# Optimization experiments

Hardware: AMD Instinct MI355X
Metric: run time of the kernel (lower is better)

Reference implementation:

```python
import jax, jax.numpy as jnp
import numpy as np

D_MODEL = 1024
N_HEADS = 16
HEAD_DIM = D_MODEL // N_HEADS  # 64
BATCH, SEQ = 2, 2048
MASK_FILL = -1000000000.0


def setup_inputs() -> dict:
    key = jax.random.key(0)
    ks = jax.random.split(key, 13)
    s = 1.0 / np.sqrt(D_MODEL)
    inp = {
        "q": jax.random.normal(ks[0], (BATCH, SEQ, D_MODEL), jnp.float32),
        "k": jax.random.normal(ks[1], (BATCH, SEQ, D_MODEL), jnp.float32),
        "v": jax.random.normal(ks[2], (BATCH, SEQ, D_MODEL), jnp.float32),
        "mask": jax.random.randint(ks[3], (BATCH, 1, SEQ, SEQ), 0, 2, jnp.int32),
        "Wq": jax.random.normal(ks[4], (D_MODEL, D_MODEL), jnp.float32) * s,
        "bq": jax.random.normal(ks[5], (D_MODEL,), jnp.float32) * s,
        "Wk": jax.random.normal(ks[6], (D_MODEL, D_MODEL), jnp.float32) * s,
        "bk": jax.random.normal(ks[7], (D_MODEL,), jnp.float32) * s,
        "Wv": jax.random.normal(ks[8], (D_MODEL, D_MODEL), jnp.float32) * s,
        "bv": jax.random.normal(ks[9], (D_MODEL,), jnp.float32) * s,
        "Wo": jax.random.normal(ks[10], (D_MODEL, D_MODEL), jnp.float32) * s,
        "bo": jax.random.normal(ks[11], (D_MODEL,), jnp.float32) * s,
    }
    return inp


def reference(q, k, v, mask, Wq, bq, Wk, bk, Wv, bv, Wo, bo):
    batch, seq, feat = q.shape
    # Linear projections (torch Linear: x @ W.T + b)
    qp = q @ Wq.T + bq
    kp = k @ Wk.T + bk
    vp = v @ Wv.T + bv

    def split(x):
        # (B, S, D) -> (B, H, S, Dh)
        return x.reshape(batch, seq, N_HEADS, HEAD_DIM).swapaxes(1, 2)

    qh, kh, vh = split(qp), split(kp), split(vp)

    # (B, H, S, S) score matrix, scaled
    score = jnp.einsum("bhqd,bhkd->bhqk", qh, kh) / jnp.sqrt(
        jnp.asarray(HEAD_DIM, qh.dtype))
    score = jnp.where(mask == 0, jnp.asarray(MASK_FILL, score.dtype), score)
    attn = jax.nn.softmax(score, axis=-1)
    out = jnp.einsum("bhqk,bhkd->bhqd", attn, vh)  # (B, H, S, Dh)
    joint = out.swapaxes(1, 2).reshape(batch, seq, feat)
    return joint @ Wo.T + bo
```

## Files before the change

### kernel.cpp

```cpp
#include <hip/hip_runtime.h>

typedef unsigned short u16;
typedef unsigned int u32;
typedef unsigned long long u64;
typedef float f32x4 __attribute__((ext_vector_type(4)));
typedef float f32x16 __attribute__((ext_vector_type(16)));
typedef __bf16 bf16x4 __attribute__((ext_vector_type(4)));
typedef __bf16 bf16x8 __attribute__((ext_vector_type(8)));
typedef u16 u16x8 __attribute__((ext_vector_type(8)));
typedef u32 u32x4 __attribute__((ext_vector_type(4)));

#define QSCALE 0.18033688011112042f

__device__ __forceinline__ u16 f2bf(float f) {
  unsigned int u = __float_as_uint(f);
  u += 0x7fffu + ((u >> 16) & 1u);
  return (u16)(u >> 16);
}

__device__ __forceinline__ void async16(const void* g, void* l) {
  __builtin_amdgcn_global_load_lds(
      (__attribute__((address_space(1))) void*)g,
      (__attribute__((address_space(3))) void*)l,
      16, 0, 0);
}

__device__ __forceinline__ f32x4 mfma16(bf16x8 a, bf16x8 b, f32x4 c) {
  return __builtin_amdgcn_mfma_f32_16x16x32_bf16(a, b, c, 0, 0, 0);
}

__device__ __forceinline__ f32x16 mfma32(bf16x8 a, bf16x8 b, f32x16 c) {
  return __builtin_amdgcn_mfma_f32_32x32x16_bf16(a, b, c, 0, 0, 0);
}

__device__ __forceinline__ u32 cvtpk(float lo, float hi) {
  u32 r;
  asm("v_cvt_pk_bf16_f32 %0, %1, %2" : "=v"(r) : "v"(lo), "v"(hi));
  return r;
}

__device__ __forceinline__ void pswap(u32& a, u32& b) {
  asm("v_permlane32_swap_b32 %0, %1" : "+v"(a), "+v"(b));
}

struct CvtArgs {
  const float* src[7];
  u16* dst[7];
};

__global__ __launch_bounds__(256) void cvt_kernel(CvtArgs a) {
  int z = blockIdx.z;
  int n = (z < 3) ? 4194304 : 1048576;
  int base = (blockIdx.x * 256 + threadIdx.x) * 8;
  if (base >= n) return;
  const float* s = a.src[z] + base;
  f32x4 x0 = *(const f32x4*)s;
  f32x4 x1 = *(const f32x4*)(s + 4);
  u16x8 pk;
  pk[0]=f2bf(x0[0]); pk[1]=f2bf(x0[1]); pk[2]=f2bf(x0[2]); pk[3]=f2bf(x0[3]);
  pk[4]=f2bf(x1[0]); pk[5]=f2bf(x1[1]); pk[6]=f2bf(x1[2]); pk[7]=f2bf(x1[3]);
  *(u16x8*)(a.dst[z] + base) = pk;
}

__global__ __launch_bounds__(256) void pack_mask_kernel(
    const int* __restrict__ mask, u64* __restrict__ pm) {
  int idx = blockIdx.x * 256 + threadIdx.x;
  const int4* src = (const int4*)(mask + (size_t)idx * 64);
  u64 bits = 0ull;
#pragma unroll
  for (int j = 0; j < 16; ++j) {
    int4 v = src[j];
    if (v.x) bits |= 1ull << (4 * j + 0);
    if (v.y) bits |= 1ull << (4 * j + 1);
    if (v.z) bits |= 1ull << (4 * j + 2);
    if (v.w) bits |= 1ull << (4 * j + 3);
  }
  pm[idx] = bits;
}

__device__ __forceinline__ void gemm_body(const u16* __restrict__ A,
                                          const u16* __restrict__ W,
                                          const float* __restrict__ bias,
                                          void* __restrict__ outraw, int mode,
                                          float oscale, int m0, int n0) {
  alignas(16) __shared__ u16 lA[128 * 32];
  alignas(16) __shared__ u16 lB[128 * 32];
  const int tid = threadIdx.x;
  const int lane = tid & 63, wv = tid >> 6;
  const int wm = wv >> 1, wn = wv & 1;
  const int l15 = lane & 15, quad = lane >> 4;
  const int srow = lane >> 2;
  const int scol = (lane & 3) * 8;

  f32x4 acc[4][4] = {};

  for (int k0 = 0; k0 < 1024; k0 += 32) {
#pragma unroll
    for (int t = 0; t < 2; ++t) {
      int rb = (wv * 2 + t) * 16;
      async16(A + (size_t)(m0 + rb + srow) * 1024 + k0 + scol, (char*)lA + rb * 64);
      async16(W + (size_t)(n0 + rb + srow) * 1024 + k0 + scol, (char*)lB + rb * 64);
    }
    __syncthreads();
    bf16x8 af[4], bfr[4];
#pragma unroll
    for (int i = 0; i < 4; ++i) {
      af[i]  = *(const bf16x8*)(lA + (wm * 64 + i * 16 + l15) * 32 + quad * 8);
      bfr[i] = *(const bf16x8*)(lB + (wn * 64 + i * 16 + l15) * 32 + quad * 8);
    }
#pragma unroll
    for (int i = 0; i < 4; ++i)
#pragma unroll
      for (int j = 0; j < 4; ++j)
        acc[i][j] = mfma16(af[i], bfr[j], acc[i][j]);
    __syncthreads();
  }

#pragma unroll
  for (int i = 0; i < 4; ++i) {
    int mbase = m0 + wm * 64 + i * 16 + quad * 4;
#pragma unroll
    for (int j = 0; j < 4; ++j) {
      int n = n0 + wn * 64 + j * 16 + l15;
      float bv = bias[n];
#pragma unroll
      for (int r = 0; r < 4; ++r) {
        int m = mbase + r;
        if (mode == 0) {
          float val = (acc[i][j][r] + bv) * oscale;
          int b = m >> 11, s = m & 2047, h = n >> 6, dh = n & 63;
          ((u16*)outraw)[((((size_t)b * 16 + h) * 2048 + s) << 6) + dh] = f2bf(val);
        } else if (mode == 1) {
          float val = (acc[i][j][r] + bias[m]) * oscale;
          int h = m >> 6, dh = m & 63, b = n >> 11, s = n & 2047;
          ((u16*)outraw)[((((size_t)b * 16 + h) * 64 + dh) << 11) + s] = f2bf(val);
        } else {
          float val = (acc[i][j][r] + bv) * oscale;
          ((float*)outraw)[(size_t)m * 1024 + n] = val;
        }
      }
    }
  }
}

__global__ __launch_bounds__(256) void gemm_qkv_kernel(
    const u16* __restrict__ qb, const u16* __restrict__ kb, const u16* __restrict__ vb,
    const u16* __restrict__ Wqb, const float* __restrict__ bq,
    const u16* __restrict__ Wkb, const float* __restrict__ bk,
    const u16* __restrict__ Wvb, const float* __restrict__ bv,
    u16* __restrict__ qp, u16* __restrict__ kp, u16* __restrict__ vt) {
  if (blockIdx.z == 0)
    gemm_body(qb, Wqb, bq, qp, 0, QSCALE, blockIdx.y * 128, blockIdx.x * 128);
  else if (blockIdx.z == 1)
    gemm_body(kb, Wkb, bk, kp, 0, 1.0f, blockIdx.y * 128, blockIdx.x * 128);
  else
    gemm_body(Wvb, vb, bv, vt, 1, 1.0f, blockIdx.x * 128, blockIdx.y * 128);
}

__global__ __launch_bounds__(256) void gemm_o_kernel(
    const u16* __restrict__ joint, const u16* __restrict__ Wob,
    const float* __restrict__ bo, float* __restrict__ out) {
  gemm_body(joint, Wob, bo, out, 2, 1.0f, blockIdx.y * 128, blockIdx.x * 128);
}

__global__ __launch_bounds__(512, 2) void attn_kernel(
    const u16* __restrict__ qp, const u16* __restrict__ kp,
    const u16* __restrict__ vt, const u64* __restrict__ pm,
    u16* __restrict__ joint) {
  alignas(16) __shared__ char smem[32768];

  const int tid = threadIdx.x, lane = tid & 63, wv = tid >> 6;
  const int l31 = lane & 31, hi = lane >> 5, l7 = lane & 7;
  const int qg = wv >> 1, kh = wv & 1;

  const int bid = blockIdx.x;
  const int grp = ((bid & 7) << 2) | ((bid >> 3) & 3);
  const int q0 = (bid >> 5) * 128;
  const int hd = grp & 15, b = grp >> 4;

  const size_t head_off = ((size_t)b * 16 + hd) * 2048 * 64;
  const u16* Qh = qp + head_off;
  const u16* Kh = kp + head_off;
  const u16* Vh = vt + head_off;
  const int qr = q0 + qg * 32 + l31;
  const u32* pmq32 = (const u32*)(pm + ((size_t)b * 2048 + qr) * 32) + kh;

  bf16x8 qf[4];
  {
    const u16* qrow = Qh + (size_t)qr * 64 + hi * 8;
#pragma unroll
    for (int d = 0; d < 4; ++d) qf[d] = *(const bf16x8*)(qrow + d * 16);
  }

  const int sd = tid;
  const int kr = sd >> 3, ks = ((sd & 7) ^ (kr & 7)) * 8;
  const u16* kg = Kh + (size_t)kr * 64 + ks;
  const u16* vg = Vh + (size_t)kr * 2048 + ks;

  f32x16 O[2] = {};
  f32x4 lacc = {};
  const f32x16 fz16 = {};

  async16(kg, smem + sd * 16);
  async16(vg, smem + 16384 + sd * 16);

  for (int kt = 0; kt < 32; ++kt) {
    __syncthreads();

    if (kt != 31) {
      const size_t kadv = (size_t)(kt + 1) * 4096;
      const int vadv = (kt + 1) * 64;
      char* kd = smem + (((kt + 1) & 1) << 13);
      char* vd = smem + 16384 + (((kt + 1) & 1) << 13);
      async16(kg + kadv, kd + sd * 16);
      async16(vg + vadv, vd + sd * 16);
    }

    u32 wh = pmq32[2 * kt];
    const char* kc = smem + ((kt & 1) << 13);
    const char* vc = smem + 16384 + ((kt & 1) << 13);

    bf16x8 kf[4];
#pragma unroll
    for (int d = 0; d < 4; ++d)
      kf[d] = *(const bf16x8*)(kc + (kh * 32 + l31) * 128 +
                               (((2 * d + hi) ^ l7) << 4));

    f32x16 S;
    {
      __builtin_amdgcn_s_setprio(1);
      f32x16 s = mfma32(kf[0], qf[0], fz16);
      s = mfma32(kf[1], qf[1], s);
      s = mfma32(kf[2], qf[2], s);
      S = mfma32(kf[3], qf[3], s);
      __builtin_amdgcn_s_setprio(0);
    }

    bf16x8 vf[2][2];
#pragma unroll
    for (int g = 0; g < 2; ++g)
#pragma unroll
      for (int t = 0; t < 2; ++t) {
        int vks = kh * 2 + t;
        vf[g][t] = *(const bf16x8*)(vc + (g * 32 + l31) * 128 +
                                    (((2 * vks + hi) ^ l7) << 4));
      }

    {
      const int hi4 = hi * 4;
#pragma unroll
      for (int rq = 0; rq < 4; ++rq) {
        u32 nib = wh >> (rq * 8 + hi4);
#pragma unroll
        for (int r4 = 0; r4 < 4; ++r4) {
          int i = rq * 4 + r4;
          float pe = __builtin_amdgcn_exp2f(S[i]);
          S[i] = ((nib >> r4) & 1u) ? pe : 0.f;
        }
        f32x4 sv = {S[rq * 4 + 0], S[rq * 4 + 1], S[rq * 4 + 2], S[rq * 4 + 3]};
        lacc += sv;
      }
    }

    bf16x8 pf[2];
#pragma unroll
    for (int t = 0; t < 2; ++t) {
      int ra = t * 8;
      u32 w0a = cvtpk(S[ra + 0], S[ra + 1]);
      u32 w1a = cvtpk(S[ra + 2], S[ra + 3]);
      u32 w0b = cvtpk(S[ra + 4], S[ra + 5]);
      u32 w1b = cvtpk(S[ra + 6], S[ra + 7]);
      pswap(w0a, w0b);
      pswap(w1a, w1b);
      u32x4 tt = {w0a, w1a, w0b, w1b};
      pf[t] = __builtin_bit_cast(bf16x8, tt);
    }

    __builtin_amdgcn_s_setprio(1);
#pragma unroll
    for (int g = 0; g < 2; ++g) {
      f32x16 o = O[g];
      o = mfma32(vf[g][0], pf[0], o);
      O[g] = mfma32(vf[g][1], pf[1], o);
    }
    __builtin_amdgcn_s_setprio(0);
  }

  float lp = (lacc[0] + lacc[1]) + (lacc[2] + lacc[3]);
  lp += __shfl_xor(lp, 32, 64);
  __syncthreads();
  float* exch = (float*)smem;
  float* e = exch + (qg * 64 + lane) * 17;
  if (kh == 1) {
#pragma unroll
    for (int i = 0; i < 16; ++i) e[i] = O[0][i];
    e[16] = lp;
  }
  __syncthreads();
  if (kh == 0) {
#pragma unroll
    for (int i = 0; i < 16; ++i) O[0][i] += e[i];
    lp += e[16];
  }
  __syncthreads();
  if (kh == 1) {
#pragma unroll
    for (int i = 0; i < 16; ++i) e[i] = O[1][i];
  }
  __syncthreads();
  if (kh == 0) {
#pragma unroll
    for (int i = 0; i < 16; ++i) O[1][i] += e[i];
    float inv = 1.0f / lp;
    size_t row_off = ((size_t)b * 2048 + qr) * 1024 + hd * 64;
#pragma unroll
    for (int g = 0; g < 2; ++g)
#pragma unroll
      for (int rq = 0; rq < 4; ++rq) {
        f32x4 ov = {O[g][rq * 4 + 0] * inv, O[g][rq * 4 + 1] * inv,
                    O[g][rq * 4 + 2] * inv, O[g][rq * 4 + 3] * inv};
        bf16x4 obv = __builtin_convertvector(ov, bf16x4);
        *(u64*)(joint + row_off + g * 32 + rq * 8 + hi * 4) =
            *(const u64*)&obv;
      }
  }
}

extern "C" void kernel_launch(void* const* d_in, const int* in_sizes, int n_in,
                              void* d_out, int out_size, void* d_ws, size_t ws_size,
                              hipStream_t stream) {
  const float* q  = (const float*)d_in[0];
  const float* k  = (const float*)d_in[1];
  const float* v  = (const float*)d_in[2];
  const int* mask = (const int*)d_in[3];
  const float* Wq = (const float*)d_in[4];
  const float* bq = (const float*)d_in[5];
  const float* Wk = (const float*)d_in[6];
  const float* bk = (const float*)d_in[7];
  const float* Wv = (const float*)d_in[8];
  const float* bv = (const float*)d_in[9];
  const float* Wo = (const float*)d_in[10];
  const float* bo = (const float*)d_in[11];
  float* out = (float*)d_out;

  u16* w = (u16*)d_ws;
  u16* qp    = w;
  u16* kp    = w + 4194304;
  u16* vt    = w + 8388608;
  u16* qb    = w + 12582912;
  u16* kb    = w + 16777216;
  u16* vb    = w + 20971520;
  u16* Wqb   = w + 25165824;
  u16* Wkb   = w + 26214400;
  u16* Wvb   = w + 27262976;
  u16* Wob   = w + 28311552;
  u64* pm    = (u64*)(w + 29360128);
  u16* joint = qb;

  CvtArgs ca;
  ca.src[0] = q;  ca.dst[0] = qb;
  ca.src[1] = k;  ca.dst[1] = kb;
  ca.src[2] = v;  ca.dst[2] = vb;
  ca.src[3] = Wq; ca.dst[3] = Wqb;
  ca.src[4] = Wk; ca.dst[4] = Wkb;
  ca.src[5] = Wv; ca.dst[5] = Wvb;
  ca.src[6] = Wo; ca.dst[6] = Wob;

  pack_mask_kernel<<<dim3(512), dim3(256), 0, stream>>>(mask, pm);
  cvt_kernel<<<dim3(2048, 1, 7), dim3(256), 0, stream>>>(ca);
  gemm_qkv_kernel<<<dim3(8, 32, 3), dim3(256), 0, stream>>>(
      qb, kb, vb, Wqb, bq, Wkb, bk, Wvb, bv, qp, kp, vt);
  attn_kernel<<<dim3(512), dim3(512), 0, stream>>>(qp, kp, vt, pm, joint);
  gemm_o_kernel<<<dim3(8, 32, 1), dim3(256), 0, stream>>>(joint, Wob, bo, out);
}
```

Measured before the change: 272.7 us.

## Fuse all stages into one cooperative persistent megakernel with grid syncs

Replaces the five separate launches (mask pack, bf16 convert, QKV GEMM, attention, output GEMM) with one cooperative kernel that runs each stage as a grid-stride loop and separates stages with grid.sync. The GEMM tile is shrunk to 128x128 per 512-thread block (each wave computes 32x64) so it matches the attention block shape. The aim is to remove per-launch overhead and inter-kernel gaps. In exchange it pays for grid barriers, gives the GEMMs 512-thread blocks with a smaller per-wave tile, and limits occupancy to what a cooperative launch allows.

```diff
diff --git a/kernel.cpp b/kernel.cpp
--- a/kernel.cpp
+++ b/kernel.cpp
@@ -1,4 +1,7 @@
 #include <hip/hip_runtime.h>
+#include <hip/hip_cooperative_groups.h>
+
+namespace cg = cooperative_groups;
 
 typedef unsigned short u16;
 typedef unsigned int u32;
@@ -43,73 +46,46 @@
   asm("v_permlane32_swap_b32 %0, %1" : "+v"(a), "+v"(b));
 }
 
-struct CvtArgs {
-  const float* src[7];
-  u16* dst[7];
+struct MegaArgs {
+  const float* csrc[7];
+  u16* cdst[7];
+  const int* mask;
+  u64* pm;
+  const float *bq, *bk, *bv, *bo;
+  u16 *qp, *kp, *vt, *joint;
+  float* out;
 };
 
-__global__ __launch_bounds__(256) void cvt_kernel(CvtArgs a) {
-  int z = blockIdx.z;
-  int n = (z < 3) ? 4194304 : 1048576;
-  int base = (blockIdx.x * 256 + threadIdx.x) * 8;
-  if (base >= n) return;
-  const float* s = a.src[z] + base;
-  f32x4 x0 = *(const f32x4*)s;
-  f32x4 x1 = *(const f32x4*)(s + 4);
-  u16x8 pk;
-  pk[0]=f2bf(x0[0]); pk[1]=f2bf(x0[1]); pk[2]=f2bf(x0[2]); pk[3]=f2bf(x0[3]);
-  pk[4]=f2bf(x1[0]); pk[5]=f2bf(x1[1]); pk[6]=f2bf(x1[2]); pk[7]=f2bf(x1[3]);
-  *(u16x8*)(a.dst[z] + base) = pk;
-}
-
-__global__ __launch_bounds__(256) void pack_mask_kernel(
-    const int* __restrict__ mask, u64* __restrict__ pm) {
-  int idx = blockIdx.x * 256 + threadIdx.x;
-  const int4* src = (const int4*)(mask + (size_t)idx * 64);
-  u64 bits = 0ull;
-#pragma unroll
-  for (int j = 0; j < 16; ++j) {
-    int4 v = src[j];
-    if (v.x) bits |= 1ull << (4 * j + 0);
-    if (v.y) bits |= 1ull << (4 * j + 1);
-    if (v.z) bits |= 1ull << (4 * j + 2);
-    if (v.w) bits |= 1ull << (4 * j + 3);
-  }
-  pm[idx] = bits;
-}
-
-__device__ __forceinline__ void gemm_body(const u16* __restrict__ A,
+__device__ __forceinline__ void gemm_tile(const u16* __restrict__ A,
                                           const u16* __restrict__ W,
                                           const float* __restrict__ bias,
                                           void* __restrict__ outraw, int mode,
-                                          float oscale, int m0, int n0) {
-  alignas(16) __shared__ u16 lA[128 * 32];
-  alignas(16) __shared__ u16 lB[128 * 32];
+                                          float oscale, int m0, int n0,
+                                          char* lds) {
+  u16* lA = (u16*)lds;
+  u16* lB = (u16*)(lds + 8192);
   const int tid = threadIdx.x;
   const int lane = tid & 63, wv = tid >> 6;
   const int wm = wv >> 1, wn = wv & 1;
   const int l15 = lane & 15, quad = lane >> 4;
-  const int srow = lane >> 2;
-  const int scol = (lane & 3) * 8;
-
-  f32x4 acc[4][4] = {};
+  const int srow = tid >> 2;
+  const int scol = (tid & 3) * 8;
+
+  f32x4 acc[2][4] = {};
 
   for (int k0 = 0; k0 < 1024; k0 += 32) {
-#pragma unroll
-    for (int t = 0; t < 2; ++t) {
-      int rb = (wv * 2 + t) * 16;
-      async16(A + (size_t)(m0 + rb + srow) * 1024 + k0 + scol, (char*)lA + rb * 64);
-      async16(W + (size_t)(n0 + rb + srow) * 1024 + k0 + scol, (char*)lB + rb * 64);
-    }
-    __syncthreads();
-    bf16x8 af[4], bfr[4];
-#pragma unroll
-    for (int i = 0; i < 4; ++i) {
-      af[i]  = *(const bf16x8*)(lA + (wm * 64 + i * 16 + l15) * 32 + quad * 8);
-      bfr[i] = *(const bf16x8*)(lB + (wn * 64 + i * 16 + l15) * 32 + quad * 8);
-    }
-#pragma unroll
-    for (int i = 0; i < 4; ++i)
+    async16(A + (size_t)(m0 + srow) * 1024 + k0 + scol, lds + tid * 16);
+    async16(W + (size_t)(n0 + srow) * 1024 + k0 + scol, lds + 8192 + tid * 16);
+    __syncthreads();
+    bf16x8 af[2], bfr[4];
+#pragma unroll
+    for (int i = 0; i < 2; ++i)
+      af[i] = *(const bf16x8*)(lA + (wm * 32 + i * 16 + l15) * 32 + quad * 8);
+#pragma unroll
+    for (int j = 0; j < 4; ++j)
+      bfr[j] = *(const bf16x8*)(lB + (wn * 64 + j * 16 + l15) * 32 + quad * 8);
+#pragma unroll
+    for (int i = 0; i < 2; ++i)
 #pragma unroll
       for (int j = 0; j < 4; ++j)
         acc[i][j] = mfma16(af[i], bfr[j], acc[i][j]);
@@ -117,8 +93,8 @@
   }
 
 #pragma unroll
-  for (int i = 0; i < 4; ++i) {
-    int mbase = m0 + wm * 64 + i * 16 + quad * 4;
+  for (int i = 0; i < 2; ++i) {
+    int mbase = m0 + wm * 32 + i * 16 + quad * 4;
 #pragma unroll
     for (int j = 0; j < 4; ++j) {
       int n = n0 + wn * 64 + j * 16 + l15;
@@ -131,11 +107,11 @@
           int b = m >> 11, s = m & 2047, h = n >> 6, dh = n & 63;
           ((u16*)outraw)[((((size_t)b * 16 + h) * 2048 + s) << 6) + dh] = f2bf(val);
         } else if (mode == 1) {
-          float val = (acc[i][j][r] + bias[m]) * oscale;
+          float val = acc[i][j][r] + bias[m];
           int h = m >> 6, dh = m & 63, b = n >> 11, s = n & 2047;
           ((u16*)outraw)[((((size_t)b * 16 + h) * 64 + dh) << 11) + s] = f2bf(val);
         } else {
-          float val = (acc[i][j][r] + bv) * oscale;
+          float val = acc[i][j][r] + bv;
           ((float*)outraw)[(size_t)m * 1024 + n] = val;
         }
       }
@@ -143,233 +119,271 @@
   }
 }
 
-__global__ __launch_bounds__(256) void gemm_qkv_kernel(
-    const u16* __restrict__ qb, const u16* __restrict__ kb, const u16* __restrict__ vb,
-    const u16* __restrict__ Wqb, const float* __restrict__ bq,
-    const u16* __restrict__ Wkb, const float* __restrict__ bk,
-    const u16* __restrict__ Wvb, const float* __restrict__ bv,
-    u16* __restrict__ qp, u16* __restrict__ kp, u16* __restrict__ vt) {
-  if (blockIdx.z == 0)
-    gemm_body(qb, Wqb, bq, qp, 0, QSCALE, blockIdx.y * 128, blockIdx.x * 128);
-  else if (blockIdx.z == 1)
-    gemm_body(kb, Wkb, bk, kp, 0, 1.0f, blockIdx.y * 128, blockIdx.x * 128);
-  else
-    gemm_body(Wvb, vb, bv, vt, 1, 1.0f, blockIdx.x * 128, blockIdx.y * 128);
-}
-
-__global__ __launch_bounds__(256) void gemm_o_kernel(
-    const u16* __restrict__ joint, const u16* __restrict__ Wob,
-    const float* __restrict__ bo, float* __restrict__ out) {
-  gemm_body(joint, Wob, bo, out, 2, 1.0f, blockIdx.y * 128, blockIdx.x * 128);
-}
-
-__global__ __launch_bounds__(512, 2) void attn_kernel(
-    const u16* __restrict__ qp, const u16* __restrict__ kp,
-    const u16* __restrict__ vt, const u64* __restrict__ pm,
-    u16* __restrict__ joint) {
+__global__ __launch_bounds__(512, 2) void mega_kernel(MegaArgs a) {
   alignas(16) __shared__ char smem[32768];
-
-  const int tid = threadIdx.x, lane = tid & 63, wv = tid >> 6;
-  const int l31 = lane & 31, hi = lane >> 5, l7 = lane & 7;
-  const int qg = wv >> 1, kh = wv & 1;
-
-  const int bid = blockIdx.x;
-  const int grp = ((bid & 7) << 2) | ((bid >> 3) & 3);
-  const int q0 = (bid >> 5) * 128;
-  const int hd = grp & 15, b = grp >> 4;
-
-  const size_t head_off = ((size_t)b * 16 + hd) * 2048 * 64;
-  const u16* Qh = qp + head_off;
-  const u16* Kh = kp + head_off;
-  const u16* Vh = vt + head_off;
-  const int qr = q0 + qg * 32 + l31;
-  const u32* pmq32 = (const u32*)(pm + ((size_t)b * 2048 + qr) * 32) + kh;
-
-  bf16x8 qf[4];
+  cg::grid_group grid = cg::this_grid();
+  const int G = gridDim.x;
+  const int tid = threadIdx.x;
+
   {
-    const u16* qrow = Qh + (size_t)qr * 64 + hi * 8;
-#pragma unroll
-    for (int d = 0; d < 4; ++d) qf[d] = *(const bf16x8*)(qrow + d * 16);
-  }
-
-  const int sd = tid;
-  const int kr = sd >> 3, ks = ((sd & 7) ^ (kr & 7)) * 8;
-  const u16* kg = Kh + (size_t)kr * 64 + ks;
-  const u16* vg = Vh + (size_t)kr * 2048 + ks;
-
-  f32x16 O[2] = {};
-  f32x4 lacc = {};
-  const f32x16 fz16 = {};
-
-  async16(kg, smem + sd * 16);
-  async16(vg, smem + 16384 + sd * 16);
-
-  for (int kt = 0; kt < 32; ++kt) {
-    __syncthreads();
-
-    if (kt != 31) {
-      const size_t kadv = (size_t)(kt + 1) * 4096;
-      const int vadv = (kt + 1) * 64;
-      char* kd = smem + (((kt + 1) & 1) << 13);
-      char* vd = smem + 16384 + (((kt + 1) & 1) << 13);
-      async16(kg + kadv, kd + sd * 16);
-      async16(vg + vadv, vd + sd * 16);
-    }
-
-    u32 wh = pmq32[2 * kt];
-    const char* kc = smem + ((kt & 1) << 13);
-    const char* vc = smem + 16384 + ((kt & 1) << 13);
-
-    bf16x8 kf[4];
-#pragma unroll
-    for (int d = 0; d < 4; ++d)
-      kf[d] = *(const bf16x8*)(kc + (kh * 32 + l31) * 128 +
-                               (((2 * d + hi) ^ l7) << 4));
-
-    f32x16 S;
+    const int gtid = blockIdx.x * 512 + tid;
+    const int gstr = G * 512;
+    for (int i = gtid; i < 2097152; i += gstr) {
+      int z, off;
+      if (i < 1572864) { z = i >> 19; off = (i & 524287) * 8; }
+      else { int j = i - 1572864; z = 3 + (j >> 17); off = (j & 131071) * 8; }
+      const float* s = a.csrc[z] + off;
+      f32x4 x0 = *(const f32x4*)s;
+      f32x4 x1 = *(const f32x4*)(s + 4);
+      u16x8 pk;
+      pk[0]=f2bf(x0[0]); pk[1]=f2bf(x0[1]); pk[2]=f2bf(x0[2]); pk[3]=f2bf(x0[3]);
+      pk[4]=f2bf(x1[0]); pk[5]=f2bf(x1[1]); pk[6]=f2bf(x1[2]); pk[7]=f2bf(x1[3]);
+      *(u16x8*)(a.cdst[z] + off) = pk;
+    }
+    for (int i = gtid; i < 131072; i += gstr) {
+      const int4* src = (const int4*)(a.mask + (size_t)i * 64);
+      u64 bits = 0ull;
+#pragma unroll
+      for (int j = 0; j < 16; ++j) {
+        int4 v = src[j];
+        if (v.x) bits |= 1ull << (4 * j + 0);
+        if (v.y) bits |= 1ull << (4 * j + 1);
+        if (v.z) bits |= 1ull << (4 * j + 2);
+        if (v.w) bits |= 1ull << (4 * j + 3);
+      }
+      a.pm[i] = bits;
+    }
+  }
+  __threadfence();
+  grid.sync();
+
+  for (int job = blockIdx.x; job < 768; job += G) {
+    int z = job >> 8, t = job & 255;
+    int my = (t >> 3) * 128, nx = (t & 7) * 128;
+    if (z == 0)
+      gemm_tile(a.cdst[0], a.cdst[3], a.bq, a.qp, 0, QSCALE, my, nx, smem);
+    else if (z == 1)
+      gemm_tile(a.cdst[1], a.cdst[4], a.bk, a.kp, 0, 1.0f, my, nx, smem);
+    else
+      gemm_tile(a.cdst[5], a.cdst[2], a.bv, a.vt, 1, 1.0f, nx, my, smem);
+  }
+  __threadfence();
+  grid.sync();
+
+  for (int bid = blockIdx.x; bid < 512; bid += G) {
+    __syncthreads();
+    const int lane = tid & 63, wv = tid >> 6;
+    const int l31 = lane & 31, hi = lane >> 5, l7 = lane & 7;
+    const int qg = wv >> 1, kh = wv & 1;
+
+    const int grp = ((bid & 7) << 2) | ((bid >> 3) & 3);
+    const int q0 = (bid >> 5) * 128;
+    const int hd = grp & 15, b = grp >> 4;
+
+    const size_t head_off = ((size_t)b * 16 + hd) * 2048 * 64;
+    const u16* Qh = a.qp + head_off;
+    const u16* Kh = a.kp + head_off;
+    const u16* Vh = a.vt + head_off;
+    const int qr = q0 + qg * 32 + l31;
+    const u32* pmq32 = (const u32*)(a.pm + ((size_t)b * 2048 + qr) * 32) + kh;
+
+    bf16x8 qf[4];
     {
+      const u16* qrow = Qh + (size_t)qr * 64 + hi * 8;
+#pragma unroll
+      for (int d = 0; d < 4; ++d) qf[d] = *(const bf16x8*)(qrow + d * 16);
+    }
+
+    const int sd = tid;
+    const int kr = sd >> 3, ks = ((sd & 7) ^ (kr & 7)) * 8;
+    const u16* kg = Kh + (size_t)kr * 64 + ks;
+    const u16* vg = Vh + (size_t)kr * 2048 + ks;
+
+    f32x16 O[2] = {};
+    f32x4 lacc = {};
+    const f32x16 fz16 = {};
+
+    async16(kg, smem + sd * 16);
+    async16(vg, smem + 16384 + sd * 16);
+
+    for (int kt = 0; kt < 32; ++kt) {
+      __syncthreads();
+
+      if (kt != 31) {
+        const size_t kadv = (size_t)(kt + 1) * 4096;
+        const int vadv = (kt + 1) * 64;
+        char* kd = smem + (((kt + 1) & 1) << 13);
+        char* vd = smem + 16384 + (((kt + 1) & 1) << 13);
+        async16(kg + kadv, kd + sd * 16);
+        async16(vg + vadv, vd + sd * 16);
+      }
+
+      u32 wh = pmq32[2 * kt];
+      const char* kc = smem + ((kt & 1) << 13);
+      const char* vc = smem + 16384 + ((kt & 1) << 13);
+
+      bf16x8 kf[4];
+#pragma unroll
+      for (int d = 0; d < 4; ++d)
+        kf[d] = *(const bf16x8*)(kc + (kh * 32 + l31) * 128 +
+                                 (((2 * d + hi) ^ l7) << 4));
+
+      f32x16 S;
+      {
+        __builtin_amdgcn_s_setprio(1);
+        f32x16 s = mfma32(kf[0], qf[0], fz16);
+        s = mfma32(kf[1], qf[1], s);
+        s = mfma32(kf[2], qf[2], s);
+        S = mfma32(kf[3], qf[3], s);
+        __builtin_amdgcn_s_setprio(0);
+      }
+
+      bf16x8 vf[2][2];
+#pragma unroll
+      for (int g = 0; g < 2; ++g)
+#pragma unroll
+        for (int t = 0; t < 2; ++t) {
+          int vks = kh * 2 + t;
+          vf[g][t] = *(const bf16x8*)(vc + (g * 32 + l31) * 128 +
+                                      (((2 * vks + hi) ^ l7) << 4));
+        }
+
+      {
+        const int hi4 = hi * 4;
+#pragma unroll
+        for (int rq = 0; rq < 4; ++rq) {
+          u32 nib = wh >> (rq * 8 + hi4);
+#pragma unroll
+          for (int r4 = 0; r4 < 4; ++r4) {
+            int i = rq * 4 + r4;
+            float pe = __builtin_amdgcn_exp2f(S[i]);
+            S[i] = ((nib >> r4) & 1u) ? pe : 0.f;
+          }
+          f32x4 sv = {S[rq * 4 + 0], S[rq * 4 + 1], S[rq * 4 + 2], S[rq * 4 + 3]};
+          lacc += sv;
+        }
+      }
+
+      bf16x8 pf[2];
+#pragma unroll
+      for (int t = 0; t < 2; ++t) {
+        int ra = t * 8;
+        u32 w0a = cvtpk(S[ra + 0], S[ra + 1]);
+        u32 w1a = cvtpk(S[ra + 2], S[ra + 3]);
+        u32 w0b = cvtpk(S[ra + 4], S[ra + 5]);
+        u32 w1b = cvtpk(S[ra + 6], S[ra + 7]);
+        pswap(w0a, w0b);
+        pswap(w1a, w1b);
+        u32x4 tt = {w0a, w1a, w0b, w1b};
+        pf[t] = __builtin_bit_cast(bf16x8, tt);
+      }
+
       __builtin_amdgcn_s_setprio(1);
-      f32x16 s = mfma32(kf[0], qf[0], fz16);
-      s = mfma32(kf[1], qf[1], s);
-      s = mfma32(kf[2], qf[2], s);
-      S = mfma32(kf[3], qf[3], s);
+#pragma unroll
+      for (int g = 0; g < 2; ++g) {
+        f32x16 o = O[g];
+        o = mfma32(vf[g][0], pf[0], o);
+        O[g] = mfma32(vf[g][1], pf[1], o);
+      }
       __builtin_amdgcn_s_setprio(0);
     }
 
-    bf16x8 vf[2][2];
-#pragma unroll
-    for (int g = 0; g < 2; ++g)
-#pragma unroll
-      for (int t = 0; t < 2; ++t) {
-        int vks = kh * 2 + t;
-        vf[g][t] = *(const bf16x8*)(vc + (g * 32 + l31) * 128 +
-                                    (((2 * vks + hi) ^ l7) << 4));
-      }
-
-    {
-      const int hi4 = hi * 4;
-#pragma unroll
-      for (int rq = 0; rq < 4; ++rq) {
-        u32 nib = wh >> (rq * 8 + hi4);
-#pragma unroll
-        for (int r4 = 0; r4 < 4; ++r4) {
-          int i = rq * 4 + r4;
-          float pe = __builtin_amdgcn_exp2f(S[i]);
-          S[i] = ((nib >> r4) & 1u) ? pe : 0.f;
+    float lp = (lacc[0] + lacc[1]) + (lacc[2] + lacc[3]);
+    lp += __shfl_xor(lp, 32, 64);
+    __syncthreads();
+    float* exch = (float*)smem;
+    float* e = exch + (qg * 64 + lane) * 17;
+    if (kh == 1) {
+#pragma unroll
+      for (int i = 0; i < 16; ++i) e[i] = O[0][i];
+      e[16] = lp;
+    }
+    __syncthreads();
+    if (kh == 0) {
+#pragma unroll
+      for (int i = 0; i < 16; ++i) O[0][i] += e[i];
+      lp += e[16];
+    }
+    __syncthreads();
+    if (kh == 1) {
+#pragma unroll
+      for (int i = 0; i < 16; ++i) e[i] = O[1][i];
+    }
+    __syncthreads();
+    if (kh == 0) {
+#pragma unroll
+      for (int i = 0; i < 16; ++i) O[1][i] += e[i];
+      float inv = 1.0f / lp;
+      size_t row_off = ((size_t)b * 2048 + qr) * 1024 + hd * 64;
+#pragma unroll
+      for (int g = 0; g < 2; ++g)
+#pragma unroll
+        for (int rq = 0; rq < 4; ++rq) {
+          f32x4 ov = {O[g][rq * 4 + 0] * inv, O[g][rq * 4 + 1] * inv,
+                      O[g][rq * 4 + 2] * inv, O[g][rq * 4 + 3] * inv};
+          bf16x4 obv = __builtin_convertvector(ov, bf16x4);
+          *(u64*)(a.joint + row_off + g * 32 + rq * 8 + hi * 4) =
+              *(const u64*)&obv;
         }
-        f32x4 sv = {S[rq * 4 + 0], S[rq * 4 + 1], S[rq * 4 + 2], S[rq * 4 + 3]};
-        lacc += sv;
-      }
-    }
-
-    bf16x8 pf[2];
-#pragma unroll
-    for (int t = 0; t < 2; ++t) {
-      int ra = t * 8;
-      u32 w0a = cvtpk(S[ra + 0], S[ra + 1]);
-      u32 w1a = cvtpk(S[ra + 2], S[ra + 3]);
-      u32 w0b = cvtpk(S[ra + 4], S[ra + 5]);
-      u32 w1b = cvtpk(S[ra + 6], S[ra + 7]);
-      pswap(w0a, w0b);
-      pswap(w1a, w1b);
-      u32x4 tt = {w0a, w1a, w0b, w1b};
-      pf[t] = __builtin_bit_cast(bf16x8, tt);
-    }
-
-    __builtin_amdgcn_s_setprio(1);
-#pragma unroll
-    for (int g = 0; g < 2; ++g) {
-      f32x16 o = O[g];
-      o = mfma32(vf[g][0], pf[0], o);
-      O[g] = mfma32(vf[g][1], pf[1], o);
-    }
-    __builtin_amdgcn_s_setprio(0);
-  }
-
-  float lp = (lacc[0] + lacc[1]) + (lacc[2] + lacc[3]);
-  lp += __shfl_xor(lp, 32, 64);
-  __syncthreads();
-  float* exch = (float*)smem;
-  float* e = exch + (qg * 64 + lane) * 17;
-  if (kh == 1) {
-#pragma unroll
-    for (int i = 0; i < 16; ++i) e[i] = O[0][i];
-    e[16] = lp;
-  }
-  __syncthreads();
-  if (kh == 0) {
-#pragma unroll
-    for (int i = 0; i < 16; ++i) O[0][i] += e[i];
-    lp += e[16];
-  }
-  __syncthreads();
-  if (kh == 1) {
-#pragma unroll
-    for (int i = 0; i < 16; ++i) e[i] = O[1][i];
-  }
-  __syncthreads();
-  if (kh == 0) {
-#pragma unroll
-    for (int i = 0; i < 16; ++i) O[1][i] += e[i];
-    float inv = 1.0f / lp;
-    size_t row_off = ((size_t)b * 2048 + qr) * 1024 + hd * 64;
-#pragma unroll
-    for (int g = 0; g < 2; ++g)
-#pragma unroll
-      for (int rq = 0; rq < 4; ++rq) {
-        f32x4 ov = {O[g][rq * 4 + 0] * inv, O[g][rq * 4 + 1] * inv,
-                    O[g][rq * 4 + 2] * inv, O[g][rq * 4 + 3] * inv};
-        bf16x4 obv = __builtin_convertvector(ov, bf16x4);
-        *(u64*)(joint + row_off + g * 32 + rq * 8 + hi * 4) =
-            *(const u64*)&obv;
-      }
+    }
+  }
+  __threadfence();
+  grid.sync();
+
+  for (int job = blockIdx.x; job < 256; job += G) {
+    __syncthreads();
+    gemm_tile(a.joint, a.cdst[6], a.bo, a.out, 2, 1.0f,
+              (job >> 3) * 128, (job & 7) * 128, smem);
   }
 }
 
 extern "C" void kernel_launch(void* const* d_in, const int* in_sizes, int n_in,
                               void* d_out, int out_size, void* d_ws, size_t ws_size,
                               hipStream_t stream) {
-  const float* q  = (const float*)d_in[0];
-  const float* k  = (const float*)d_in[1];
-  const float* v  = (const float*)d_in[2];
-  const int* mask = (const int*)d_in[3];
-  const float* Wq = (const float*)d_in[4];
-  const float* bq = (const float*)d_in[5];
-  const float* Wk = (const float*)d_in[6];
-  const float* bk = (const float*)d_in[7];
-  const float* Wv = (const float*)d_in[8];
-  const float* bv = (const float*)d_in[9];
-  const float* Wo = (const float*)d_in[10];
-  const float* bo = (const float*)d_in[11];
-  float* out = (float*)d_out;
-
   u16* w = (u16*)d_ws;
-  u16* qp    = w;
-  u16* kp    = w + 4194304;
-  u16* vt    = w + 8388608;
-  u16* qb    = w + 12582912;
-  u16* kb    = w + 16777216;
-  u16* vb    = w + 20971520;
-  u16* Wqb   = w + 25165824;
-  u16* Wkb   = w + 26214400;
-  u16* Wvb   = w + 27262976;
-  u16* Wob   = w + 28311552;
-  u64* pm    = (u64*)(w + 29360128);
-  u16* joint = qb;
-
-  CvtArgs ca;
-  ca.src[0] = q;  ca.dst[0] = qb;
-  ca.src[1] = k;  ca.dst[1] = kb;
-  ca.src[2] = v;  ca.dst[2] = vb;
-  ca.src[3] = Wq; ca.dst[3] = Wqb;
-  ca.src[4] = Wk; ca.dst[4] = Wkb;
-  ca.src[5] = Wv; ca.dst[5] = Wvb;
-  ca.src[6] = Wo; ca.dst[6] = Wob;
-
-  pack_mask_kernel<<<dim3(512), dim3(256), 0, stream>>>(mask, pm);
-  cvt_kernel<<<dim3(2048, 1, 7), dim3(256), 0, stream>>>(ca);
-  gemm_qkv_kernel<<<dim3(8, 32, 3), dim3(256), 0, stream>>>(
-      qb, kb, vb, Wqb, bq, Wkb, bk, Wvb, bv, qp, kp, vt);
-  attn_kernel<<<dim3(512), dim3(512), 0, stream>>>(qp, kp, vt, pm, joint);
-  gemm_o_kernel<<<dim3(8, 32, 1), dim3(256), 0, stream>>>(joint, Wob, bo, out);
-}
+
+  MegaArgs ma;
+  ma.csrc[0] = (const float*)d_in[0];
+  ma.csrc[1] = (const float*)d_in[1];
+  ma.csrc[2] = (const float*)d_in[2];
+  ma.csrc[3] = (const float*)d_in[4];
+  ma.csrc[4] = (const float*)d_in[6];
+  ma.csrc[5] = (const float*)d_in[8];
+  ma.csrc[6] = (const float*)d_in[10];
+  ma.mask = (const int*)d_in[3];
+  ma.bq = (const float*)d_in[5];
+  ma.bk = (const float*)d_in[7];
+  ma.bv = (const float*)d_in[9];
+  ma.bo = (const float*)d_in[11];
+
+  ma.qp = w;
+  ma.kp = w + 4194304;
+  ma.vt = w + 8388608;
+  ma.cdst[0] = w + 12582912;
+  ma.cdst[1] = w + 16777216;
+  ma.cdst[2] = w + 20971520;
+  ma.cdst[3] = w + 25165824;
+  ma.cdst[4] = w + 26214400;
+  ma.cdst[5] = w + 27262976;
+  ma.cdst[6] = w + 28311552;
+  ma.pm = (u64*)(w + 29360128);
+  ma.joint = ma.cdst[0];
+  ma.out = (float*)d_out;
+
+  static int nblk = 0;
+  if (nblk == 0) {
+    int per_cu = 0;
+    if (hipOccupancyMaxActiveBlocksPerMultiprocessor(&per_cu, mega_kernel,
+                                                     512, 0) == hipSuccess &&
+        per_cu >= 1) {
+      nblk = per_cu * 256;
+      if (nblk > 512) nblk = 512;
+    } else {
+      nblk = 256;
+    }
+  }
+
+  void* kargs[] = {(void*)&ma};
+  hipLaunchCooperativeKernel((const void*)mega_kernel, dim3(nblk), dim3(512),
+                             kargs, 0, stream);
+}
```

Result: slower. 609.5 us (+123.5%).

## Widen GEMM K-step to 64 with XOR-swizzled LDS and grouped tile order

Applied to the files above, without the earlier changes.

The GEMM main loop now loads a 64-wide K slice per iteration instead of 32. This halves the number of barrier pairs and doubles the MFMA work done between them. LDS rows are XOR-swizzled to avoid bank conflicts on the wider 128-byte rows. Blocks are remapped so that consecutive block IDs share weight tiles, for better L2 reuse. The change doubles GEMM LDS usage, which may reduce occupancy. It also drops the redundant oscale multiplies where oscale is always 1.

```diff
diff --git a/kernel.cpp b/kernel.cpp
--- a/kernel.cpp
+++ b/kernel.cpp
@@ -83,36 +83,49 @@
                                           const float* __restrict__ bias,
                                           void* __restrict__ outraw, int mode,
                                           float oscale, int m0, int n0) {
-  alignas(16) __shared__ u16 lA[128 * 32];
-  alignas(16) __shared__ u16 lB[128 * 32];
+  alignas(16) __shared__ u16 lA[128 * 64];
+  alignas(16) __shared__ u16 lB[128 * 64];
   const int tid = threadIdx.x;
   const int lane = tid & 63, wv = tid >> 6;
   const int wm = wv >> 1, wn = wv & 1;
   const int l15 = lane & 15, quad = lane >> 4;
-  const int srow = lane >> 2;
-  const int scol = (lane & 3) * 8;
+  const int xsw = l15 & 7;
+
+  int srow[4], scol[4];
+#pragma unroll
+  for (int t = 0; t < 4; ++t) {
+    int slot = t * 256 + tid;
+    srow[t] = slot >> 3;
+    scol[t] = ((slot & 7) ^ (srow[t] & 7)) * 8;
+  }
 
   f32x4 acc[4][4] = {};
 
-  for (int k0 = 0; k0 < 1024; k0 += 32) {
-#pragma unroll
-    for (int t = 0; t < 2; ++t) {
-      int rb = (wv * 2 + t) * 16;
-      async16(A + (size_t)(m0 + rb + srow) * 1024 + k0 + scol, (char*)lA + rb * 64);
-      async16(W + (size_t)(n0 + rb + srow) * 1024 + k0 + scol, (char*)lB + rb * 64);
+  for (int k0 = 0; k0 < 1024; k0 += 64) {
+#pragma unroll
+    for (int t = 0; t < 4; ++t) {
+      int slot = t * 256 + tid;
+      async16(A + (size_t)(m0 + srow[t]) * 1024 + k0 + scol[t],
+              (char*)lA + slot * 16);
+      async16(W + (size_t)(n0 + srow[t]) * 1024 + k0 + scol[t],
+              (char*)lB + slot * 16);
     }
     __syncthreads();
-    bf16x8 af[4], bfr[4];
-#pragma unroll
-    for (int i = 0; i < 4; ++i) {
-      af[i]  = *(const bf16x8*)(lA + (wm * 64 + i * 16 + l15) * 32 + quad * 8);
-      bfr[i] = *(const bf16x8*)(lB + (wn * 64 + i * 16 + l15) * 32 + quad * 8);
-    }
-#pragma unroll
-    for (int i = 0; i < 4; ++i)
-#pragma unroll
-      for (int j = 0; j < 4; ++j)
-        acc[i][j] = mfma16(af[i], bfr[j], acc[i][j]);
+#pragma unroll
+    for (int ks = 0; ks < 2; ++ks) {
+      bf16x8 af[4], bfr[4];
+#pragma unroll
+      for (int i = 0; i < 4; ++i) {
+        int c = ((ks * 4 + quad) ^ xsw) * 8;
+        af[i]  = *(const bf16x8*)(lA + (wm * 64 + i * 16 + l15) * 64 + c);
+        bfr[i] = *(const bf16x8*)(lB + (wn * 64 + i * 16 + l15) * 64 + c);
+      }
+#pragma unroll
+      for (int i = 0; i < 4; ++i)
+#pragma unroll
+        for (int j = 0; j < 4; ++j)
+          acc[i][j] = mfma16(af[i], bfr[j], acc[i][j]);
+    }
     __syncthreads();
   }
 
@@ -131,16 +144,21 @@
           int b = m >> 11, s = m & 2047, h = n >> 6, dh = n & 63;
           ((u16*)outraw)[((((size_t)b * 16 + h) * 2048 + s) << 6) + dh] = f2bf(val);
         } else if (mode == 1) {
-          float val = (acc[i][j][r] + bias[m]) * oscale;
+          float val = acc[i][j][r] + bias[m];
           int h = m >> 6, dh = m & 63, b = n >> 11, s = n & 2047;
           ((u16*)outraw)[((((size_t)b * 16 + h) * 64 + dh) << 11) + s] = f2bf(val);
         } else {
-          float val = (acc[i][j][r] + bv) * oscale;
+          float val = acc[i][j][r] + bv;
           ((float*)outraw)[(size_t)m * 1024 + n] = val;
         }
       }
     }
   }
+}
+
+__device__ __forceinline__ void tile_map(int t, int& mt, int& nt) {
+  mt = (t & 7) * 4 + ((t >> 3) & 3);
+  nt = t >> 5;
 }
 
 __global__ __launch_bounds__(256) void gemm_qkv_kernel(
@@ -149,18 +167,22 @@
     const u16* __restrict__ Wkb, const float* __restrict__ bk,
     const u16* __restrict__ Wvb, const float* __restrict__ bv,
     u16* __restrict__ qp, u16* __restrict__ kp, u16* __restrict__ vt) {
-  if (blockIdx.z == 0)
-    gemm_body(qb, Wqb, bq, qp, 0, QSCALE, blockIdx.y * 128, blockIdx.x * 128);
-  else if (blockIdx.z == 1)
-    gemm_body(kb, Wkb, bk, kp, 0, 1.0f, blockIdx.y * 128, blockIdx.x * 128);
+  int mt, nt;
+  tile_map(blockIdx.x, mt, nt);
+  if (blockIdx.y == 0)
+    gemm_body(qb, Wqb, bq, qp, 0, QSCALE, mt * 128, nt * 128);
+  else if (blockIdx.y == 1)
+    gemm_body(kb, Wkb, bk, kp, 0, 1.0f, mt * 128, nt * 128);
   else
-    gemm_body(Wvb, vb, bv, vt, 1, 1.0f, blockIdx.x * 128, blockIdx.y * 128);
+    gemm_body(Wvb, vb, bv, vt, 1, 1.0f, nt * 128, mt * 128);
 }
 
 __global__ __launch_bounds__(256) void gemm_o_kernel(
     const u16* __restrict__ joint, const u16* __restrict__ Wob,
     const float* __restrict__ bo, float* __restrict__ out) {
-  gemm_body(joint, Wob, bo, out, 2, 1.0f, blockIdx.y * 128, blockIdx.x * 128);
+  int mt, nt;
+  tile_map(blockIdx.x, mt, nt);
+  gemm_body(joint, Wob, bo, out, 2, 1.0f, mt * 128, nt * 128);
 }
 
 __global__ __launch_bounds__(512, 2) void attn_kernel(
@@ -368,8 +390,8 @@
 
   pack_mask_kernel<<<dim3(512), dim3(256), 0, stream>>>(mask, pm);
   cvt_kernel<<<dim3(2048, 1, 7), dim3(256), 0, stream>>>(ca);
-  gemm_qkv_kernel<<<dim3(8, 32, 3), dim3(256), 0, stream>>>(
+  gemm_qkv_kernel<<<dim3(256, 3), dim3(256), 0, stream>>>(
       qb, kb, vb, Wqb, bq, Wkb, bk, Wvb, bv, qp, kp, vt);
   attn_kernel<<<dim3(512), dim3(512), 0, stream>>>(qp, kp, vt, pm, joint);
-  gemm_o_kernel<<<dim3(8, 32, 1), dim3(256), 0, stream>>>(joint, Wob, bo, out);
-}
+  gemm_o_kernel<<<dim3(256), dim3(256), 0, stream>>>(joint, Wob, bo, out);
+}
```

New measurement: 263.4 us. -3.4%, faster.
